# Kernel tuning notes

Hardware: AMD Instinct MI355X
Metric: run time of the kernel (lower is better)

The kernel has to match this reference:

```python
import jax, jax.numpy as jnp
import numpy as np

N_NODES = 50000
N_EDGES = 800000
IN_DIM = 128
EMB = 64
EDGE_DIM = 6
N_LAYERS = 4
OUT_DIM = 1


def setup_inputs() -> dict:
    key = jax.random.key(0)
    ks = jax.random.split(key, 20)
    s = 0.05
    inp = {
        "x": jax.random.normal(ks[0], (N_NODES, IN_DIM), jnp.float32),
        "edge_index": jax.random.randint(ks[1], (2, N_EDGES), 0, N_NODES, jnp.int64),
        "edge_attr": jax.random.normal(ks[2], (N_EDGES, EDGE_DIM), jnp.float32),
        # input projection
        "lin_in_w": jax.random.normal(ks[3], (IN_DIM, EMB), jnp.float32) * s,
        "lin_in_b": jnp.zeros((EMB,), jnp.float32),
        # stacked per-layer MLP params: message MLP psi: (2*EMB+EDGE_DIM)->EMB->EMB
        "msg_w1": jax.random.normal(ks[4], (N_LAYERS, 2 * EMB + EDGE_DIM, EMB), jnp.float32) * s,
        "msg_b1": jnp.zeros((N_LAYERS, EMB), jnp.float32),
        "msg_w2": jax.random.normal(ks[5], (N_LAYERS, EMB, EMB), jnp.float32) * s,
        "msg_b2": jnp.zeros((N_LAYERS, EMB), jnp.float32),
        # update MLP phi: (2*EMB)->EMB->EMB
        "upd_w1": jax.random.normal(ks[6], (N_LAYERS, 2 * EMB, EMB), jnp.float32) * s,
        "upd_b1": jnp.zeros((N_LAYERS, EMB), jnp.float32),
        "upd_w2": jax.random.normal(ks[7], (N_LAYERS, EMB, EMB), jnp.float32) * s,
        "upd_b2": jnp.zeros((N_LAYERS, EMB), jnp.float32),
        # output head
        "pred_w": jax.random.normal(ks[8], (EMB, OUT_DIM), jnp.float32) * s,
        "pred_b": jnp.zeros((OUT_DIM,), jnp.float32),
    }
    return inp


def reference(x, edge_index, edge_attr, lin_in_w, lin_in_b,
              msg_w1, msg_b1, msg_w2, msg_b2,
              upd_w1, upd_b1, upd_w2, upd_b2,
              pred_w, pred_b):
    n = x.shape[0]
    src = edge_index[0]  # h_j: source nodes
    dst = edge_index[1]  # h_i: target nodes (aggregation index in PyG default flow)
    h = x @ lin_in_w + lin_in_b  # (n, EMB)
    n_layers = msg_w1.shape[0]
    for l in range(n_layers):
        # message: psi([h_i, h_j, e_ij])  -> (E, EMB)
        m = jnp.concatenate([h[dst], h[src], edge_attr], axis=-1)
        m = jax.nn.relu(m @ msg_w1[l] + msg_b1[l])
        m = jax.nn.relu(m @ msg_w2[l] + msg_b2[l])
        # aggregate: scatter-add over target nodes
        agg = jax.ops.segment_sum(m, dst, num_segments=n)
        # update: phi([h, m_i]) with residual connection (h = h + conv(h))
        u = jnp.concatenate([h, agg], axis=-1)
        u = jax.nn.relu(u @ upd_w1[l] + upd_b1[l])
        u = jax.nn.relu(u @ upd_w2[l] + upd_b2[l])
        h = h + u
    out = h @ pred_w + pred_b  # (n, OUT_DIM)
    return jnp.sum(out, axis=-2)  # (OUT_DIM,)
```

## Files before the change

kernel.cpp:

```cpp
#include <hip/hip_runtime.h>
#include <hip/hip_fp16.h>


typedef __attribute__((ext_vector_type(8))) short short8;
typedef __attribute__((ext_vector_type(4))) float float4v;

__device__ __forceinline__ unsigned short f2bf(float f) {
    unsigned int u = __float_as_uint(f);
    unsigned int r = u + 0x7fff + ((u >> 16) & 1);
    return (unsigned short)(r >> 16);
}
__device__ __forceinline__ float bf2f(unsigned short u) {
    return __uint_as_float(((unsigned int)u) << 16);
}
__device__ __forceinline__ __half2 u2h2(unsigned int u) {
    union { unsigned int u; __half2 h; } c; c.u = u; return c.h;
}
__device__ __forceinline__ unsigned int h22u(__half2 h) {
    union { unsigned int u; __half2 h; } c; c.h = h; return c.u;
}
__device__ __forceinline__ unsigned int pkmax0(unsigned int a) {
    unsigned int r;
    asm("v_pk_max_f16 %0, %1, %2" : "=v"(r) : "v"(a), "v"(0u));
    return r;
}

#define MFMA16(a, b, c)  __builtin_amdgcn_mfma_f32_16x16x32_bf16(a, b, c, 0, 0, 0)
#define MFMA16H(a, b, c) __builtin_amdgcn_mfma_f32_16x16x32_f16(a, b, c, 0, 0, 0)

struct bfpair { short hi, lo; };
__device__ __forceinline__ bfpair wsplit(float wv) {
    bfpair p;
    unsigned short h = f2bf(wv);
    float hf = __uint_as_float(((unsigned int)h) << 16);
    p.hi = (short)h;
    p.lo = (short)f2bf(wv - hf);
    return p;
}

#define WP_TOTAL 106496
#define OFF_IN   0
#define OFF_PRE(l)  (8192  + (l) * 8192)
#define OFF_MW2(l)  (40960 + (l) * 4096)
#define OFF_UW1(l)  (57344 + (l) * 8192)
#define OFF_UW2(l)  (90112 + (l) * 4096)

__global__ __launch_bounds__(256) void k_wprep(const float* __restrict__ lin_w,
        const float* __restrict__ mw1, const float* __restrict__ mw2,
        const float* __restrict__ uw1, const float* __restrict__ uw2,
        unsigned short* __restrict__ H, unsigned short* __restrict__ L) {
    const int tid = blockIdx.x * 256 + threadIdx.x;
    if (tid >= WP_TOTAL) return;
    float val;
    if (tid < 8192) {
        int rem = tid;
        int nt = rem >> 11, kf = (rem >> 9) & 3;
        int lane = (rem >> 3) & 63, j = rem & 7;
        int k = kf * 32 + (lane >> 4) * 8 + j;
        val = lin_w[k * 64 + nt * 16 + (lane & 15)];
    } else if (tid < 40960) {
        int t = tid - 8192, layer = t >> 13, rem = t & 8191;
        int nt = rem >> 10, kf = (rem >> 9) & 1;
        int lane = (rem >> 3) & 63, j = rem & 7;
        int k = kf * 32 + (lane >> 4) * 8 + j;
        const float* w1 = mw1 + (size_t)layer * 134 * 64;
        val = (nt < 4) ? w1[k * 64 + nt * 16 + (lane & 15)]
                       : w1[(64 + k) * 64 + (nt - 4) * 16 + (lane & 15)];
    } else if (tid < 57344) {
        int t = tid - 40960, layer = t >> 12, rem = t & 4095;
        int nt = rem >> 10, kf = (rem >> 9) & 1;
        int lane = (rem >> 3) & 63, j = rem & 7;
        int k = kf * 32 + (lane >> 4) * 8 + j;
        val = mw2[(size_t)layer * 4096 + k * 64 + nt * 16 + (lane & 15)];
    } else if (tid < 90112) {
        int t = tid - 57344, layer = t >> 13, rem = t & 8191;
        int nt = rem >> 11, kf = (rem >> 9) & 3;
        int lane = (rem >> 3) & 63, j = rem & 7;
        int k = kf * 32 + (lane >> 4) * 8 + j;
        val = uw1[(size_t)layer * 8192 + k * 64 + nt * 16 + (lane & 15)];
    } else {
        int t = tid - 90112, layer = t >> 12, rem = t & 4095;
        int nt = rem >> 10, kf = (rem >> 9) & 1;
        int lane = (rem >> 3) & 63, j = rem & 7;
        int k = kf * 32 + (lane >> 4) * 8 + j;
        val = uw2[(size_t)layer * 4096 + k * 64 + nt * 16 + (lane & 15)];
    }
    if (tid >= 40960 && tid < 57344) {
        __half hh = __float2half_rn(val);
        float hf = __half2float(hh);
        __half hl = __float2half_rn(val - hf);
        H[tid] = __half_as_ushort(hh);
        L[tid] = __half_as_ushort(hl);
    } else {
        bfpair p = wsplit(val);
        H[tid] = (unsigned short)p.hi;
        L[tid] = (unsigned short)p.lo;
    }
}

#define LOADFRAG(dst, arr, nt, KF, kf) \
    dst = *(const short8*)&arr[((((nt) * (KF)) + (kf)) * 64 + lane) * 8]

__global__ __launch_bounds__(256) void k_hist(const int* __restrict__ dst,
        int* __restrict__ deg, int nEdges) {
    int e = blockIdx.x * blockDim.x + threadIdx.x;
    if (e < nEdges) atomicAdd(&deg[dst[e]], 1);
}

__global__ __launch_bounds__(256) void k_scan1(const int* __restrict__ deg,
        int* __restrict__ local, int* __restrict__ bsum, int nNodes) {
    __shared__ int sm[256];
    const int t = threadIdx.x;
    const int n = blockIdx.x * 256 + t;
    int v = (n < nNodes) ? deg[n] : 0;
    sm[t] = v;
    __syncthreads();
    for (int off = 1; off < 256; off <<= 1) {
        int u = (t >= off) ? sm[t - off] : 0;
        __syncthreads();
        sm[t] += u;
        __syncthreads();
    }
    if (n < nNodes) local[n] = sm[t] - v;
    if (t == 255) bsum[blockIdx.x] = sm[255];
}

__global__ __launch_bounds__(256) void k_scan2(int* __restrict__ bsum, int nB) {
    __shared__ int sm[256];
    const int t = threadIdx.x;
    int v = (t < nB) ? bsum[t] : 0;
    sm[t] = v;
    __syncthreads();
    for (int off = 1; off < 256; off <<= 1) {
        int u = (t >= off) ? sm[t - off] : 0;
        __syncthreads();
        sm[t] += u;
        __syncthreads();
    }
    if (t < nB) bsum[t] = sm[t] - v;
}

__global__ __launch_bounds__(256) void k_scan3(const int* __restrict__ local,
        const int* __restrict__ bsum, int* __restrict__ cursor, int nNodes) {
    int n = blockIdx.x * 256 + threadIdx.x;
    if (n < nNodes) cursor[n] = bsum[blockIdx.x] + local[n];
}

__global__ __launch_bounds__(256) void k_scatter(const int* __restrict__ src,
        const int* __restrict__ dst, const float* __restrict__ ea,
        int* __restrict__ cursor, float* __restrict__ rec, int nEdges) {
    int e = blockIdx.x * blockDim.x + threadIdx.x;
    if (e < nEdges) {
        int d = dst[e];
        int s = src[e];
        int pos = atomicAdd(&cursor[d], 1);
        const float* p = ea + (size_t)e * 6;
        float4 lo, hi;
        lo.x = __int_as_float(s);
        lo.y = __int_as_float(d);
        lo.z = p[0];
        lo.w = p[1];
        hi.x = p[2];
        hi.y = p[3];
        hi.z = p[4];
        hi.w = p[5];
        float4* q = (float4*)(rec + (size_t)pos * 8);
        q[0] = lo;
        q[1] = hi;
    }
}


__global__ __launch_bounds__(256) void k_in(const float* __restrict__ x,
        const unsigned short* __restrict__ wh, const unsigned short* __restrict__ wl,
        const float* __restrict__ bia, float* __restrict__ h, int nNodes) {
    const int lane = threadIdx.x & 63;
    const int wib  = threadIdx.x >> 6;
    const int quad = lane >> 4, col = lane & 15;
    __shared__ unsigned short sm[4][16 * 136];
    unsigned short* __restrict__ mt = sm[wib];

    short8 bh[4][4], bl[4][4];
#pragma unroll
    for (int nt = 0; nt < 4; ++nt)
#pragma unroll
        for (int kf = 0; kf < 4; ++kf) {
            LOADFRAG(bh[nt][kf], wh, nt, 4, kf);
            LOADFRAG(bl[nt][kf], wl, nt, 4, kf);
        }
    float bv[4];
#pragma unroll
    for (int nt = 0; nt < 4; ++nt) bv[nt] = bia[nt * 16 + col];

    const int nTiles = (nNodes + 15) >> 4;
    const int wid = blockIdx.x * 4 + wib;
    const int nw  = gridDim.x * 4;
    for (int tile = wid; tile < nTiles; tile += nw) {
        const int base = tile * 16;
#pragma unroll
        for (int j = 0; j < 16; ++j) {
            int row = min(base + j, nNodes - 1);
            mt[j * 136 + lane]      = f2bf(x[(size_t)row * 128 + lane]);
            mt[j * 136 + 64 + lane] = f2bf(x[(size_t)row * 128 + 64 + lane]);
        }
        __builtin_amdgcn_s_waitcnt(0);
        short8 a[4];
#pragma unroll
        for (int kf = 0; kf < 4; ++kf)
            a[kf] = *(const short8*)&mt[col * 136 + kf * 32 + quad * 8];
#pragma unroll
        for (int nt = 0; nt < 4; ++nt) {
            float4v c = {0.f, 0.f, 0.f, 0.f};
#pragma unroll
            for (int kf = 0; kf < 4; ++kf) c = MFMA16(a[kf], bh[nt][kf], c);
#pragma unroll
            for (int kf = 0; kf < 4; ++kf) c = MFMA16(a[kf], bl[nt][kf], c);
#pragma unroll
            for (int r = 0; r < 4; ++r) {
                int row = base + quad * 4 + r;
                if (row < nNodes)
                    h[(size_t)row * 64 + nt * 16 + col] = c[r] + bv[nt];
            }
        }
    }
}

__global__ __launch_bounds__(256) void k_pre(const float* __restrict__ h,
        const unsigned short* __restrict__ wh, const unsigned short* __restrict__ wl,
        const float* __restrict__ b1m,
        unsigned short* __restrict__ P, unsigned short* __restrict__ Q,
        int nNodes) {
    const int lane = threadIdx.x & 63;
    const int wib  = threadIdx.x >> 6;
    const int quad = lane >> 4, col = lane & 15;
    __shared__ unsigned short sm[4][16 * 72];
    unsigned short* __restrict__ mt = sm[wib];

    short8 bh[8][2], bl[8][2];
#pragma unroll
    for (int nt = 0; nt < 8; ++nt)
#pragma unroll
        for (int kf = 0; kf < 2; ++kf) {
            LOADFRAG(bh[nt][kf], wh, nt, 2, kf);
            LOADFRAG(bl[nt][kf], wl, nt, 2, kf);
        }
    float bv1[4];
#pragma unroll
    for (int nt = 0; nt < 4; ++nt) bv1[nt] = b1m[nt * 16 + col];

    const int nTiles = (nNodes + 15) >> 4;
    const int wid = blockIdx.x * 4 + wib;
    const int nw  = gridDim.x * 4;
    for (int tile = wid; tile < nTiles; tile += nw) {
        const int base = tile * 16;
#pragma unroll
        for (int j = 0; j < 16; ++j) {
            int row = min(base + j, nNodes - 1);
            mt[j * 72 + lane] = f2bf(h[(size_t)row * 64 + lane]);
        }
        __builtin_amdgcn_s_waitcnt(0);
        short8 a0 = *(const short8*)&mt[col * 72 + quad * 8];
        short8 a1 = *(const short8*)&mt[col * 72 + 32 + quad * 8];
#pragma unroll
        for (int nt = 0; nt < 8; ++nt) {
            float4v c = {0.f, 0.f, 0.f, 0.f};
            c = MFMA16(a0, bh[nt][0], c);
            c = MFMA16(a1, bh[nt][1], c);
            c = MFMA16(a0, bl[nt][0], c);
            c = MFMA16(a1, bl[nt][1], c);
            unsigned short* __restrict__ outp = (nt < 4) ? P : Q;
            const int nc = (nt & 3) * 16 + col;
            const float badd = (nt < 4) ? bv1[nt & 3] : 0.f;
#pragma unroll
            for (int r = 0; r < 4; ++r) {
                int row = base + quad * 4 + r;
                if (row < nNodes)
                    outp[(size_t)row * 64 + nc] =
                        __half_as_ushort(__float2half_rn(c[r] + badd));
            }
        }
    }
}

__global__ __launch_bounds__(256) void k_upd(float* __restrict__ h,
        float* __restrict__ agg,
        const unsigned short* __restrict__ wh1, const unsigned short* __restrict__ wl1,
        const float* __restrict__ b1,
        const unsigned short* __restrict__ wh2, const unsigned short* __restrict__ wl2,
        const float* __restrict__ b2, float* __restrict__ colsum,
        int nNodes, int doCS) {
    const int lane = threadIdx.x & 63;
    const int wib  = threadIdx.x >> 6;
    const int quad = lane >> 4, col = lane & 15;
    __shared__ unsigned short sm[4][16 * 136];
    __shared__ unsigned short tb[4][16 * 72];
    __shared__ unsigned short wB[8192];
    unsigned short* __restrict__ mt = sm[wib];
    unsigned short* __restrict__ tv = tb[wib];

    {
        const short8* __restrict__ sH = (const short8*)wh2;
        const short8* __restrict__ sL = (const short8*)wl2;
        short8* __restrict__ dB = (short8*)wB;
        for (int i = threadIdx.x; i < 512; i += 256) {
            dB[i]       = sH[i];
            dB[512 + i] = sL[i];
        }
    }
    __syncthreads();

    short8 bh[4][4], bl[4][4];
#pragma unroll
    for (int nt = 0; nt < 4; ++nt)
#pragma unroll
        for (int kf = 0; kf < 4; ++kf) {
            LOADFRAG(bh[nt][kf], wh1, nt, 4, kf);
            LOADFRAG(bl[nt][kf], wl1, nt, 4, kf);
        }
    float bv1[4], bv2[4];
#pragma unroll
    for (int nt = 0; nt < 4; ++nt) {
        bv1[nt] = b1[nt * 16 + col];
        bv2[nt] = b2[nt * 16 + col];
    }

    float cs0 = 0.f, cs1 = 0.f, cs2 = 0.f, cs3 = 0.f;
    const int nTiles = (nNodes + 15) >> 4;
    const int wid = blockIdx.x * 4 + wib;
    const int nw  = gridDim.x * 4;
    for (int tile = wid; tile < nTiles; tile += nw) {
        const int base = tile * 16;
#pragma unroll
        for (int j = 0; j < 16; ++j) {
            int row = min(base + j, nNodes - 1);
            mt[j * 136 + lane]      = f2bf(h[(size_t)row * 64 + lane]);
            mt[j * 136 + 64 + lane] = f2bf(agg[(size_t)row * 64 + lane]);
        }
        __builtin_amdgcn_s_waitcnt(0);
#pragma unroll
        for (int j = 0; j < 16; ++j) {
            int row = base + j;
            if (row < nNodes) agg[(size_t)row * 64 + lane] = 0.f;
        }
        short8 a[4];
#pragma unroll
        for (int kf = 0; kf < 4; ++kf)
            a[kf] = *(const short8*)&mt[col * 136 + kf * 32 + quad * 8];
#pragma unroll
        for (int nt = 0; nt < 4; ++nt) {
            float4v c = {0.f, 0.f, 0.f, 0.f};
#pragma unroll
            for (int kf = 0; kf < 4; ++kf) c = MFMA16(a[kf], bh[nt][kf], c);
#pragma unroll
            for (int kf = 0; kf < 4; ++kf) c = MFMA16(a[kf], bl[nt][kf], c);
#pragma unroll
            for (int r = 0; r < 4; ++r)
                tv[(quad * 4 + r) * 72 + nt * 16 + col] =
                    f2bf(fmaxf(c[r] + bv1[nt], 0.f));
        }
        __builtin_amdgcn_s_waitcnt(0);
        short8 a0 = *(const short8*)&tv[col * 72 + quad * 8];
        short8 a1 = *(const short8*)&tv[col * 72 + 32 + quad * 8];
#pragma unroll
        for (int nt = 0; nt < 4; ++nt) {
            const short8 h0 = *(const short8*)&wB[((nt * 2 + 0) * 64 + lane) * 8];
            const short8 h1 = *(const short8*)&wB[((nt * 2 + 1) * 64 + lane) * 8];
            const short8 l0 = *(const short8*)&wB[4096 + ((nt * 2 + 0) * 64 + lane) * 8];
            const short8 l1 = *(const short8*)&wB[4096 + ((nt * 2 + 1) * 64 + lane) * 8];
            float4v c = {0.f, 0.f, 0.f, 0.f};
            c = MFMA16(a0, h0, c);
            c = MFMA16(a1, h1, c);
            c = MFMA16(a0, l0, c);
            c = MFMA16(a1, l1, c);
#pragma unroll
            for (int r = 0; r < 4; ++r) {
                int row = base + quad * 4 + r;
                if (row < nNodes) {
                    float* hp = &h[(size_t)row * 64 + nt * 16 + col];
                    float hn = *hp + fmaxf(c[r] + bv2[nt], 0.f);
                    *hp = hn;
                    cs0 += (nt == 0) ? hn : 0.f;
                    cs1 += (nt == 1) ? hn : 0.f;
                    cs2 += (nt == 2) ? hn : 0.f;
                    cs3 += (nt == 3) ? hn : 0.f;
                }
            }
        }
    }
    if (doCS) {
        cs0 += __shfl_xor(cs0, 16); cs0 += __shfl_xor(cs0, 32);
        cs1 += __shfl_xor(cs1, 16); cs1 += __shfl_xor(cs1, 32);
        cs2 += __shfl_xor(cs2, 16); cs2 += __shfl_xor(cs2, 32);
        cs3 += __shfl_xor(cs3, 16); cs3 += __shfl_xor(cs3, 32);
        const float tot = (quad == 0) ? cs0 : (quad == 1) ? cs1
                        : (quad == 2) ? cs2 : cs3;
        atomicAdd(&colsum[lane], tot);
    }
}

#define EST 72

__global__ __launch_bounds__(256, 4) void k_edge(const unsigned short* __restrict__ P,
        const unsigned short* __restrict__ Q, const float* __restrict__ rec,
        const float* __restrict__ w1e,
        const unsigned short* __restrict__ wh, const unsigned short* __restrict__ wl,
        const float* __restrict__ b2,
        float* __restrict__ agg, int nEdges) {
    const int lane = threadIdx.x & 63;
    const int wib  = threadIdx.x >> 6;
    const int wid  = blockIdx.x * 4 + wib;
    const int nw   = gridDim.x * 4;
    const int quad = lane >> 4;
    const int col  = lane & 15;
    const int li   = lane & 31;
    const int hs   = lane >> 5;

    __shared__ unsigned short m1b[4][32 * EST];
    __shared__ unsigned int   eab[4][256];
    __shared__ unsigned short wB[8192];
    unsigned short* __restrict__ mt  = m1b[wib];
    unsigned int*   __restrict__ eaw = eab[wib];

    {
        const short8* __restrict__ sH = (const short8*)wh;
        const short8* __restrict__ sL = (const short8*)wl;
        short8* __restrict__ dB = (short8*)wB;
        for (int i = threadIdx.x; i < 512; i += 256) {
            dB[i]       = sH[i];
            dB[512 + i] = sL[i];
        }
    }
    __syncthreads();

    __half2 w1ec2[6];
#pragma unroll
    for (int jj = 0; jj < 6; ++jj)
        w1ec2[jj] = __halves2half2(__float2half_rn(w1e[jj * 64 + 2 * li]),
                                   __float2half_rn(w1e[jj * 64 + 2 * li + 1]));

    float b2v[4];
#pragma unroll
    for (int nt = 0; nt < 4; ++nt) b2v[nt] = b2[nt * 16 + col];

    const int nBatch = (nEdges + 31) >> 5;
    const int per = nBatch / nw, rem = nBatch % nw;
    const int btLo = wid * per + min(wid, rem);
    const int btHi = btLo + per + (wid < rem ? 1 : 0);

    const int* __restrict__ reci = (const int*)rec;

    for (int bt = btLo; bt < btHi; ++bt) {
        const int base = __builtin_amdgcn_readfirstlane(bt << 5);
        const int gidx = min(base + li, nEdges - 1);
        const int vsj = reci[(size_t)gidx * 8];
        const int vdj = reci[(size_t)gidx * 8 + 1];
        const int vprev = __shfl_up(vdj, 1);
        unsigned long long bmask =
            __ballot(lane < 32 && (li == 0 || vdj != vprev));
        bmask |= (1ull << 32) | 1ull;

        const int fMax = nEdges * 8 - 1;
        const int fBase = base * 8;
#pragma unroll
        for (int k = 0; k < 4; ++k)
            eaw[k * 64 + lane] =
                h22u(__float2half2_rn(rec[min(fBase + k * 64 + lane, fMax)]));

#pragma unroll
        for (int j = 0; j < 16; ++j) {
            const int d0 = __builtin_amdgcn_readlane(vdj, 2 * j);
            const int d1 = __builtin_amdgcn_readlane(vdj, 2 * j + 1);
            const int s0 = __builtin_amdgcn_readlane(vsj, 2 * j);
            const int s1 = __builtin_amdgcn_readlane(vsj, 2 * j + 1);
            const int d = hs ? d1 : d0;
            const int s = hs ? s1 : s0;
            const int rsel = 2 * j + hs;
            const unsigned int p2 = *(const unsigned int*)&P[(size_t)d * 64 + 2 * li];
            const unsigned int q2 = *(const unsigned int*)&Q[(size_t)s * 64 + 2 * li];
            __half2 t = __hadd2(u2h2(p2), u2h2(q2));
#pragma unroll
            for (int jj = 0; jj < 6; ++jj) {
                const unsigned int eu = eaw[16 * j + 8 * hs + 2 + jj];
                t = __hfma2(u2h2(eu), w1ec2[jj], t);
            }
            *(unsigned int*)((char*)mt + rsel * (EST * 2) + li * 4) = pkmax0(h22u(t));
        }
        __builtin_amdgcn_s_waitcnt(0);

        short8 a00 = *(const short8*)&mt[col * EST + quad * 8];
        short8 a01 = *(const short8*)&mt[col * EST + 32 + quad * 8];
        short8 a10 = *(const short8*)&mt[(16 + col) * EST + quad * 8];
        short8 a11 = *(const short8*)&mt[(16 + col) * EST + 32 + quad * 8];

        float4v m2v[2][4];
#pragma unroll
        for (int nt = 0; nt < 4; ++nt) {
            const short8 h0 = *(const short8*)&wB[((nt * 2 + 0) * 64 + lane) * 8];
            const short8 h1 = *(const short8*)&wB[((nt * 2 + 1) * 64 + lane) * 8];
            const short8 l0 = *(const short8*)&wB[4096 + ((nt * 2 + 0) * 64 + lane) * 8];
            const short8 l1 = *(const short8*)&wB[4096 + ((nt * 2 + 1) * 64 + lane) * 8];
            float4v c0 = {0.f, 0.f, 0.f, 0.f};
            float4v c1 = {0.f, 0.f, 0.f, 0.f};
            c0 = MFMA16H(a00, h0, c0);
            c0 = MFMA16H(a01, h1, c0);
            c0 = MFMA16H(a00, l0, c0);
            c0 = MFMA16H(a01, l1, c0);
            c1 = MFMA16H(a10, h0, c1);
            c1 = MFMA16H(a11, h1, c1);
            c1 = MFMA16H(a10, l0, c1);
            c1 = MFMA16H(a11, l1, c1);
#pragma unroll
            for (int r = 0; r < 4; ++r) {
                const bool v0 = base + (quad * 4 + r) < nEdges;
                const bool v1 = base + 16 + (quad * 4 + r) < nEdges;
                m2v[0][nt][r] = v0 ? fmaxf(c0[r] + b2v[nt], 0.f) : 0.f;
                m2v[1][nt][r] = v1 ? fmaxf(c1[r] + b2v[nt], 0.f) : 0.f;
            }
        }

        int r0 = 0;
        while (r0 < 32) {
            const int nid = __builtin_amdgcn_readlane(vdj, r0);
            const int r1 = r0 + 1 + (int)__builtin_ctzll(bmask >> (r0 + 1));
            float s0 = 0.f, s1 = 0.f, s2 = 0.f, s3 = 0.f;
#pragma unroll
            for (int t = 0; t < 2; ++t)
#pragma unroll
                for (int r = 0; r < 4; ++r) {
                    const int R = t * 16 + quad * 4 + r;
                    const bool in = (R >= r0) && (R < r1);
                    s0 += in ? m2v[t][0][r] : 0.f;
                    s1 += in ? m2v[t][1][r] : 0.f;
                    s2 += in ? m2v[t][2][r] : 0.f;
                    s3 += in ? m2v[t][3][r] : 0.f;
                }
            s0 += __shfl_xor(s0, 16); s0 += __shfl_xor(s0, 32);
            s1 += __shfl_xor(s1, 16); s1 += __shfl_xor(s1, 32);
            s2 += __shfl_xor(s2, 16); s2 += __shfl_xor(s2, 32);
            s3 += __shfl_xor(s3, 16); s3 += __shfl_xor(s3, 32);
            const float tot = (quad == 0) ? s0 : (quad == 1) ? s1
                            : (quad == 2) ? s2 : s3;
            atomicAdd(&agg[(size_t)nid * 64 + lane], tot);
            r0 = r1;
        }
    }
}

__global__ void k_out(const float* __restrict__ colsum, const float* __restrict__ pw,
                      const float* __restrict__ pb, float* __restrict__ out, int nNodes) {
    const int lane = threadIdx.x;
    float v = colsum[lane] * pw[lane];
#pragma unroll
    for (int off = 32; off; off >>= 1) v += __shfl_down(v, off);
    if (lane == 0) out[0] = v + (float)nNodes * pb[0];
}

extern "C" void kernel_launch(void* const* d_in, const int* in_sizes, int n_in,
                              void* d_out, int out_size, void* d_ws, size_t ws_size,
                              hipStream_t stream) {
    const float* x     = (const float*)d_in[0];
    const int*   ei    = (const int*)d_in[1];
    const float* ea    = (const float*)d_in[2];
    const float* lin_w = (const float*)d_in[3];
    const float* lin_b = (const float*)d_in[4];
    const float* mw1   = (const float*)d_in[5];
    const float* mb1   = (const float*)d_in[6];
    const float* mw2   = (const float*)d_in[7];
    const float* mb2   = (const float*)d_in[8];
    const float* uw1   = (const float*)d_in[9];
    const float* ub1   = (const float*)d_in[10];
    const float* uw2   = (const float*)d_in[11];
    const float* ub2   = (const float*)d_in[12];
    const float* pw    = (const float*)d_in[13];
    const float* pb    = (const float*)d_in[14];

    const int nNodes = in_sizes[0] / 128;
    const int nEdges = in_sizes[1] / 2;
    const int* src = ei;
    const int* dst = ei + nEdges;

    float* h       = (float*)d_ws;
    float* agg     = h   + (size_t)nNodes * 64;
    float* rec     = agg + (size_t)nNodes * 64;
    float* colsum  = rec + (size_t)nEdges * 8;
    unsigned short* Pb  = (unsigned short*)(colsum + 64);
    unsigned short* Qb  = Pb + (size_t)nNodes * 64;
    unsigned short* wpH = Qb + (size_t)nNodes * 64;
    unsigned short* wpL = wpH + WP_TOTAL;
    int*   deg     = (int*)(wpL + WP_TOTAL);
    int*   cursor  = deg + nNodes;
    int*   local   = cursor + nNodes;
    int*   bsum    = local + nNodes;

    const int NB_T    = 392;
    const int NB_EDGE = 2048;
    const int NB_FLAT = (nEdges + 255) / 256;
    const int NB_SCAN = (nNodes + 255) / 256;

    hipMemsetAsync(deg, 0, (size_t)nNodes * sizeof(int), stream);
    hipMemsetAsync(colsum, 0, 64 * sizeof(float), stream);
    hipMemsetAsync(agg, 0, (size_t)nNodes * 64 * sizeof(float), stream);
    k_hist<<<NB_FLAT, 256, 0, stream>>>(dst, deg, nEdges);
    k_scan1<<<NB_SCAN, 256, 0, stream>>>(deg, local, bsum, nNodes);
    k_scan2<<<1, 256, 0, stream>>>(bsum, NB_SCAN);
    k_scan3<<<NB_SCAN, 256, 0, stream>>>(local, bsum, cursor, nNodes);
    k_scatter<<<NB_FLAT, 256, 0, stream>>>(src, dst, ea, cursor, rec, nEdges);
    k_wprep<<<(WP_TOTAL + 255) / 256, 256, 0, stream>>>(lin_w, mw1, mw2, uw1, uw2, wpH, wpL);

    k_in<<<NB_T, 256, 0, stream>>>(x, wpH + OFF_IN, wpL + OFF_IN, lin_b, h, nNodes);

    for (int l = 0; l < 4; ++l) {
        k_pre<<<NB_T, 256, 0, stream>>>(h, wpH + OFF_PRE(l), wpL + OFF_PRE(l),
            mb1 + l * 64, Pb, Qb, nNodes);
        k_edge<<<NB_EDGE, 256, 0, stream>>>(Pb, Qb, rec,
            mw1 + (size_t)l * 134 * 64 + 128 * 64,
            wpH + OFF_MW2(l), wpL + OFF_MW2(l), mb2 + l * 64, agg, nEdges);
        k_upd<<<NB_T, 256, 0, stream>>>(h, agg,
            wpH + OFF_UW1(l), wpL + OFF_UW1(l), ub1 + l * 64,
            wpH + OFF_UW2(l), wpL + OFF_UW2(l), ub2 + l * 64,
            colsum, nNodes, (l == 3) ? 1 : 0);
    }

    k_out<<<1, 64, 0, stream>>>(colsum, pw, pb, (float*)d_out, nNodes);
}
```

Measured before the change: 538.0 us.

## Fuse next layer's P/Q precompute into the node update kernel

The per-layer k_pre launch, which reread h to compute the P/Q projections for the edge kernel, is folded into k_upd. The freshly updated h tile is staged in LDS as fp16 and multiplied against the next layer's pre-weights. This removes three kernel launches and one full read of h per layer. In exchange it adds 16KB of LDS per block, which may lower occupancy, and the pre-weights are now rounded to fp16 rather than kept as a hi/lo bf16 split, which may change accuracy.

```diff
diff --git a/kernel.cpp b/kernel.cpp
--- a/kernel.cpp
+++ b/kernel.cpp
@@ -287,14 +287,19 @@
         const unsigned short* __restrict__ wh1, const unsigned short* __restrict__ wl1,
         const float* __restrict__ b1,
         const unsigned short* __restrict__ wh2, const unsigned short* __restrict__ wl2,
-        const float* __restrict__ b2, float* __restrict__ colsum,
-        int nNodes, int doCS) {
+        const float* __restrict__ b2,
+        const unsigned short* __restrict__ whP, const unsigned short* __restrict__ wlP,
+        const float* __restrict__ b1m,
+        unsigned short* __restrict__ P, unsigned short* __restrict__ Q,
+        float* __restrict__ colsum,
+        int nNodes, int doCS, int doPre) {
     const int lane = threadIdx.x & 63;
     const int wib  = threadIdx.x >> 6;
     const int quad = lane >> 4, col = lane & 15;
     __shared__ unsigned short sm[4][16 * 136];
     __shared__ unsigned short tb[4][16 * 72];
     __shared__ unsigned short wB[8192];
+    __shared__ unsigned short wP[8192];
     unsigned short* __restrict__ mt = sm[wib];
     unsigned short* __restrict__ tv = tb[wib];
 
@@ -306,6 +311,21 @@
             dB[i]       = sH[i];
             dB[512 + i] = sL[i];
         }
+        if (doPre) {
+            const short8* __restrict__ pH = (const short8*)whP;
+            const short8* __restrict__ pL = (const short8*)wlP;
+            short8* __restrict__ dP = (short8*)wP;
+            for (int i = threadIdx.x; i < 1024; i += 256) {
+                short8 hi8 = pH[i], lo8 = pL[i], o;
+#pragma unroll
+                for (int e = 0; e < 8; ++e) {
+                    float w = bf2f((unsigned short)hi8[e]) +
+                              bf2f((unsigned short)lo8[e]);
+                    o[e] = (short)__half_as_ushort(__float2half_rn(w));
+                }
+                dP[i] = o;
+            }
+        }
     }
     __syncthreads();
 
@@ -317,11 +337,12 @@
             LOADFRAG(bh[nt][kf], wh1, nt, 4, kf);
             LOADFRAG(bl[nt][kf], wl1, nt, 4, kf);
         }
-    float bv1[4], bv2[4];
+    float bv1[4], bv2[4], bvP[4];
 #pragma unroll
     for (int nt = 0; nt < 4; ++nt) {
         bv1[nt] = b1[nt * 16 + col];
         bv2[nt] = b2[nt * 16 + col];
+        bvP[nt] = b1m[nt * 16 + col];
     }
 
     float cs0 = 0.f, cs1 = 0.f, cs2 = 0.f, cs3 = 0.f;
@@ -379,10 +400,36 @@
                     float* hp = &h[(size_t)row * 64 + nt * 16 + col];
                     float hn = *hp + fmaxf(c[r] + bv2[nt], 0.f);
                     *hp = hn;
+                    if (doPre)
+                        tv[(quad * 4 + r) * 72 + nt * 16 + col] =
+                            __half_as_ushort(__float2half_rn(hn));
                     cs0 += (nt == 0) ? hn : 0.f;
                     cs1 += (nt == 1) ? hn : 0.f;
                     cs2 += (nt == 2) ? hn : 0.f;
                     cs3 += (nt == 3) ? hn : 0.f;
+                }
+            }
+        }
+        if (doPre) {
+            __builtin_amdgcn_s_waitcnt(0);
+            short8 p0 = *(const short8*)&tv[col * 72 + quad * 8];
+            short8 p1 = *(const short8*)&tv[col * 72 + 32 + quad * 8];
+#pragma unroll
+            for (int nt = 0; nt < 8; ++nt) {
+                const short8 f0 = *(const short8*)&wP[((nt * 2 + 0) * 64 + lane) * 8];
+                const short8 f1 = *(const short8*)&wP[((nt * 2 + 1) * 64 + lane) * 8];
+                float4v c = {0.f, 0.f, 0.f, 0.f};
+                c = MFMA16H(p0, f0, c);
+                c = MFMA16H(p1, f1, c);
+                unsigned short* __restrict__ outp = (nt < 4) ? P : Q;
+                const int nc = (nt & 3) * 16 + col;
+                const float badd = (nt < 4) ? bvP[nt & 3] : 0.f;
+#pragma unroll
+                for (int r = 0; r < 4; ++r) {
+                    int row = base + quad * 4 + r;
+                    if (row < nNodes)
+                        outp[(size_t)row * 64 + nc] =
+                            __half_as_ushort(__float2half_rn(c[r] + badd));
                 }
             }
         }
@@ -608,17 +655,20 @@
     k_wprep<<<(WP_TOTAL + 255) / 256, 256, 0, stream>>>(lin_w, mw1, mw2, uw1, uw2, wpH, wpL);
 
     k_in<<<NB_T, 256, 0, stream>>>(x, wpH + OFF_IN, wpL + OFF_IN, lin_b, h, nNodes);
+    k_pre<<<NB_T, 256, 0, stream>>>(h, wpH + OFF_PRE(0), wpL + OFF_PRE(0),
+        mb1, Pb, Qb, nNodes);
 
     for (int l = 0; l < 4; ++l) {
-        k_pre<<<NB_T, 256, 0, stream>>>(h, wpH + OFF_PRE(l), wpL + OFF_PRE(l),
-            mb1 + l * 64, Pb, Qb, nNodes);
+        const int lp = (l < 3) ? (l + 1) : 3;
         k_edge<<<NB_EDGE, 256, 0, stream>>>(Pb, Qb, rec,
             mw1 + (size_t)l * 134 * 64 + 128 * 64,
             wpH + OFF_MW2(l), wpL + OFF_MW2(l), mb2 + l * 64, agg, nEdges);
         k_upd<<<NB_T, 256, 0, stream>>>(h, agg,
             wpH + OFF_UW1(l), wpL + OFF_UW1(l), ub1 + l * 64,
             wpH + OFF_UW2(l), wpL + OFF_UW2(l), ub2 + l * 64,
-            colsum, nNodes, (l == 3) ? 1 : 0);
+            wpH + OFF_PRE(lp), wpL + OFF_PRE(lp),
+            (l < 3) ? (mb1 + (l + 1) * 64) : mb1,
+            Pb, Qb, colsum, nNodes, (l == 3) ? 1 : 0, (l < 3) ? 1 : 0);
     }
 
     k_out<<<1, 64, 0, stream>>>(colsum, pw, pb, (float*)d_out, nNodes);
```

Measured after the change: 526.1 us. 2.2% less time.
